# Performance work log

Measured on AMD Instinct MI355X. Metric: run time of the kernel, lower is better.

## Reference

```python
import jax, jax.numpy as jnp
import numpy as np

B, S, D, H, F = 8, 1024, 768, 12, 3072
DH = D // H
C_QUAD = 5.0
LN_EPS = 1e-5


def layer_norm(x, g, b):
    mu = jnp.mean(x, axis=-1, keepdims=True)
    var = jnp.mean(jnp.square(x - mu), axis=-1, keepdims=True)
    return (x - mu) * jax.lax.rsqrt(var + LN_EPS) * g + b


def setup_inputs() -> dict:
    key = jax.random.key(0)
    ks = jax.random.split(key, 8)
    s_in = 1.0 / np.sqrt(D)
    s_ff = 1.0 / np.sqrt(F)
    return {
        "x": jax.random.normal(ks[0], (B, S, D), jnp.float32),
        "wqkv": jax.random.normal(ks[1], (D, 3 * D), jnp.float32) * s_in,
        "bqkv": jnp.zeros((3 * D,), jnp.float32),
        "wo": jax.random.normal(ks[2], (D, D), jnp.float32) * s_in,
        "bo": jnp.zeros((D,), jnp.float32),
        "ln1_g": jnp.ones((D,), jnp.float32),
        "ln1_b": jnp.zeros((D,), jnp.float32),
        "w1": jax.random.normal(ks[3], (D, F), jnp.float32) * s_in,
        "b1": jnp.zeros((F,), jnp.float32),
        "w2": jax.random.normal(ks[4], (F, D), jnp.float32) * s_ff,
        "b2": jnp.zeros((D,), jnp.float32),
        "ln2_g": jnp.ones((D,), jnp.float32),
        "ln2_b": jnp.zeros((D,), jnp.float32),
    }


def quad2(scores):
    # Quad2 custom 'softmax': (s + c)^2 normalized by row sum
    s2 = jnp.square(scores + C_QUAD)
    return s2 / jnp.sum(s2, axis=-1, keepdims=True)


def reference(x, wqkv, bqkv, wo, bo, ln1_g, ln1_b, w1, b1, w2, b2, ln2_g, ln2_b):
    # --- pre-norm multi-head attention with Quad2 score normalization ---
    h = layer_norm(x, ln1_g, ln1_b)
    qkv = h @ wqkv + bqkv                              # [B,S,3D]
    q, k, v = jnp.split(qkv, 3, axis=-1)
    q = q.reshape(B, S, H, DH).transpose(0, 2, 1, 3)   # [B,H,S,Dh]
    k = k.reshape(B, S, H, DH).transpose(0, 2, 1, 3)
    v = v.reshape(B, S, H, DH).transpose(0, 2, 1, 3)
    scale = 1.0 / np.sqrt(DH)
    scores = jnp.einsum("bhqd,bhkd->bhqk", q, k) * scale
    attn = quad2(scores)                               # [B,H,S,S]
    ctx = jnp.einsum("bhqk,bhkd->bhqd", attn, v)
    ctx = ctx.transpose(0, 2, 1, 3).reshape(B, S, D)
    x = x + ctx @ wo + bo
    # --- pre-norm FFN ---
    h = layer_norm(x, ln2_g, ln2_b)
    h = jax.nn.gelu(h @ w1 + b1)
    x = x + h @ w2 + b2
    return x
```

## Files before the change

kernel.cpp:

```cpp
#include <hip/hip_runtime.h>
#include <hip/hip_bf16.h>

constexpr int B_ = 8;
constexpr int S_ = 1024;
constexpr int D_ = 768;
constexpr int H_ = 12;
constexpr int F_ = 3072;
constexpr int DH_ = 64;
constexpr int M_ = B_ * S_;
constexpr int PSZ = B_ * S_ * D_;

typedef __bf16 bf16x8 __attribute__((ext_vector_type(8)));
typedef float f32x4 __attribute__((ext_vector_type(4)));
typedef short s16x8 __attribute__((ext_vector_type(8)));
typedef short s16x4 __attribute__((ext_vector_type(4)));

__device__ __forceinline__ void gload_lds16(const __bf16* g, __bf16* l) {
    __builtin_amdgcn_global_load_lds(
        (const __attribute__((address_space(1))) void*)g,
        (__attribute__((address_space(3))) void*)l,
        16, 0, 0);
}

__device__ __forceinline__ float fast_gelu(float x) {
    float x3 = x * x * x;
    float z = 0.7978845608028654f * x + 0.035677408136300125f * x3;
    float e = __builtin_amdgcn_exp2f(-2.8853900817779268f * z);
    return x * __builtin_amdgcn_rcpf(1.0f + e);
}

__global__ __launch_bounds__(256) void transpose_cvt(const float* __restrict__ in,
                                                     __bf16* __restrict__ out,
                                                     int K, int N) {
    __shared__ float t[32][33];
    int tx = threadIdx.x, ty = threadIdx.y;
    int n0 = blockIdx.x * 32, k0 = blockIdx.y * 32;
#pragma unroll
    for (int i = 0; i < 4; ++i)
        t[ty + i * 8][tx] = in[(size_t)(k0 + ty + i * 8) * N + n0 + tx];
    __syncthreads();
#pragma unroll
    for (int i = 0; i < 4; ++i)
        out[(size_t)(n0 + ty + i * 8) * K + k0 + tx] = (__bf16)t[tx][ty + i * 8];
}

__global__ __launch_bounds__(256) void ln_kernel(const float* __restrict__ x,
                                                 const float* __restrict__ g,
                                                 const float* __restrict__ bb,
                                                 __bf16* __restrict__ out) {
    int row = blockIdx.x;
    const float* xr = x + (size_t)row * D_;
    int tid = threadIdx.x;
    float v[3];
    float s = 0.f, s2 = 0.f;
#pragma unroll
    for (int j = 0; j < 3; ++j) {
        v[j] = xr[tid + j * 256];
        s += v[j];
        s2 += v[j] * v[j];
    }
#pragma unroll
    for (int o = 32; o >= 1; o >>= 1) {
        s += __shfl_xor(s, o, 64);
        s2 += __shfl_xor(s2, o, 64);
    }
    __shared__ float red[8];
    int wid = tid >> 6, lane = tid & 63;
    if (lane == 0) { red[wid] = s; red[4 + wid] = s2; }
    __syncthreads();
    s = red[0] + red[1] + red[2] + red[3];
    s2 = red[4] + red[5] + red[6] + red[7];
    float mu = s * (1.0f / D_);
    float var = s2 * (1.0f / D_) - mu * mu;
    float rs = rsqrtf(var + 1e-5f);
    __bf16* orow = out + (size_t)row * D_;
#pragma unroll
    for (int j = 0; j < 3; ++j) {
        int i = tid + j * 256;
        orow[i] = (__bf16)((v[j] - mu) * rs * g[i] + bb[i]);
    }
}

template <int EPI>
__device__ __forceinline__ void gemm4_body(const __bf16* __restrict__ A,
                                           const __bf16* __restrict__ Bt,
                                           const float* __restrict__ bias,
                                           const float* __restrict__ res,
                                           float* __restrict__ outf,
                                           __bf16* __restrict__ outb,
                                           int M, int N, int K) {
    __shared__ __bf16 lds[2][16384];

    const int tid = threadIdx.x;
    const int lane = tid & 63, wid = tid >> 6;
    const int wm = wid >> 1, wn = wid & 1;
    const int gx = gridDim.x;
    const int nwg = gx * gridDim.y;
    int flat = blockIdx.y * gx + blockIdx.x;
    flat = (flat & 7) * (nwg >> 3) + (flat >> 3);
    const int bm = (flat / gx) * 128, bn = (flat % gx) * 128;
    const int l15 = lane & 15, l4 = lane >> 4;
    f32x4 acc[4][4] = {};

    const int r8 = tid >> 3;
    const int swc = ((tid & 7) ^ (r8 & 7)) * 8;
    const __bf16* ga = A + (size_t)(bm + r8) * K + swc;
    const __bf16* gb = Bt + (size_t)(bn + r8) * K + swc;
    const int NT = K / 64;

    auto stage = [&](int t, int s) {
        const int kt = t * 64;
        __bf16* base = &lds[s][0] + tid * 8;
#pragma unroll
        for (int j = 0; j < 4; ++j)
            gload_lds16(ga + kt + (size_t)j * 32 * K, base + j * 2048);
#pragma unroll
        for (int j = 0; j < 4; ++j)
            gload_lds16(gb + kt + (size_t)j * 32 * K, base + 8192 + j * 2048);
    };

    stage(0, 0);
    for (int t = 0; t < NT; ++t) {
        if (t + 1 < NT) {
            stage(t + 1, (t + 1) & 1);
            asm volatile("s_waitcnt vmcnt(8)" ::: "memory");
        } else {
            asm volatile("s_waitcnt vmcnt(0)" ::: "memory");
        }
        asm volatile("s_barrier" ::: "memory");

        const __bf16* sA = &lds[t & 1][0];
        const __bf16* sB = sA + 8192;
        const int swr = (l15 & 7) * 8;
        bf16x8 a[4][2], b[4][2];
#pragma unroll
        for (int mf = 0; mf < 4; ++mf) {
            int row = wm * 64 + mf * 16 + l15;
#pragma unroll
            for (int ks = 0; ks < 2; ++ks)
                a[mf][ks] = *(const bf16x8*)&sA[row * 64 + ((ks * 32 + l4 * 8) ^ swr)];
        }
#pragma unroll
        for (int nf = 0; nf < 4; ++nf) {
            int row = wn * 64 + nf * 16 + l15;
#pragma unroll
            for (int ks = 0; ks < 2; ++ks)
                b[nf][ks] = *(const bf16x8*)&sB[row * 64 + ((ks * 32 + l4 * 8) ^ swr)];
        }
        asm volatile("s_waitcnt lgkmcnt(0)" ::: "memory");
        asm volatile("s_barrier" ::: "memory");
        __builtin_amdgcn_sched_barrier(0);

        __builtin_amdgcn_s_setprio(1);
#pragma unroll
        for (int ks = 0; ks < 2; ++ks)
#pragma unroll
            for (int mf = 0; mf < 4; ++mf)
#pragma unroll
                for (int nf = 0; nf < 4; ++nf)
                    acc[mf][nf] = __builtin_amdgcn_mfma_f32_16x16x32_bf16(
                        a[mf][ks], b[nf][ks], acc[mf][nf], 0, 0, 0);
        __builtin_amdgcn_s_setprio(0);
    }

    if constexpr (EPI == 0) {
#pragma unroll
        for (int nf = 0; nf < 4; ++nf) {
            int n = bn + wn * 64 + nf * 16 + l15;
            int part = n / 768;
            int n7 = n - part * 768;
            float bv = bias[n];
            size_t obase = (size_t)part * PSZ + (size_t)(n7 >> 6) * (S_ * DH_) + (n7 & 63);
#pragma unroll
            for (int mf = 0; mf < 4; ++mf) {
                int m0 = bm + wm * 64 + mf * 16 + l4 * 4;
                size_t rb = obase + (size_t)(m0 >> 10) * ((size_t)H_ * S_ * DH_) +
                            (size_t)(m0 & 1023) * DH_;
#pragma unroll
                for (int r = 0; r < 4; ++r)
                    outb[rb + (size_t)r * DH_] = (__bf16)(acc[mf][nf][r] + bv);
            }
        }
    } else {
#pragma unroll
        for (int mf = 0; mf < 4; ++mf) {
#pragma unroll
            for (int nf = 0; nf < 4; ++nf) {
#pragma unroll
                for (int r = 0; r < 4; ++r) {
                    int m = bm + wm * 64 + mf * 16 + l4 * 4 + r;
                    int n = bn + wn * 64 + nf * 16 + l15;
                    float val = acc[mf][nf][r] + bias[n];
                    if constexpr (EPI == 1) {
                        outf[(size_t)m * N + n] = val + res[(size_t)m * N + n];
                    } else {
                        outb[(size_t)m * N + n] = (__bf16)fast_gelu(val);
                    }
                }
            }
        }
    }
}

template <int EPI>
__device__ __forceinline__ void gemmk_body(const __bf16* __restrict__ A,
                                           const __bf16* __restrict__ Bt,
                                           const float* __restrict__ bias,
                                           const float* __restrict__ res,
                                           float* __restrict__ outf,
                                           __bf16* __restrict__ outb,
                                           int M, int N, int K) {
    __shared__ __bf16 lds[2][16384];

    const int tid = threadIdx.x;
    const int lane = tid & 63, wid = tid >> 6;
    const int wm = wid >> 2, wn = wid & 3;
    const int gx = gridDim.x;
    const int nwg = gx * gridDim.y;
    int flat = blockIdx.y * gx + blockIdx.x;
    flat = (flat & 7) * (nwg >> 3) + (flat >> 3);
    const int bm = (flat / gx) * 128, bn = (flat % gx) * 128;
    const int l15 = lane & 15, l4 = lane >> 4;
    f32x4 acc[4][2] = {};

    const int r8 = tid >> 3;
    const int swc = ((tid & 7) ^ (r8 & 7)) * 8;
    const __bf16* ga = A + (size_t)(bm + r8) * K + swc;
    const __bf16* gb = Bt + (size_t)(bn + r8) * K + swc;
    const int NT = K / 64;

    auto stage = [&](int t, int s) {
        const int kt = t * 64;
        __bf16* base = &lds[s][0] + tid * 8;
        gload_lds16(ga + kt, base);
        gload_lds16(ga + kt + (size_t)64 * K, base + 4096);
        gload_lds16(gb + kt, base + 8192);
        gload_lds16(gb + kt + (size_t)64 * K, base + 12288);
    };

    stage(0, 0);
    for (int t = 0; t < NT; ++t) {
        if (t + 1 < NT) {
            stage(t + 1, (t + 1) & 1);
            asm volatile("s_waitcnt vmcnt(4)" ::: "memory");
        } else {
            asm volatile("s_waitcnt vmcnt(0)" ::: "memory");
        }
        asm volatile("s_barrier" ::: "memory");

        const __bf16* sA = &lds[t & 1][0];
        const __bf16* sB = sA + 8192;
        const int swr = (l15 & 7) * 8;
        bf16x8 a[4][2], b[2][2];
#pragma unroll
        for (int mf = 0; mf < 4; ++mf) {
            int row = wm * 64 + mf * 16 + l15;
#pragma unroll
            for (int ks = 0; ks < 2; ++ks)
                a[mf][ks] = *(const bf16x8*)&sA[row * 64 + ((ks * 32 + l4 * 8) ^ swr)];
        }
#pragma unroll
        for (int nf = 0; nf < 2; ++nf) {
            int row = wn * 32 + nf * 16 + l15;
#pragma unroll
            for (int ks = 0; ks < 2; ++ks)
                b[nf][ks] = *(const bf16x8*)&sB[row * 64 + ((ks * 32 + l4 * 8) ^ swr)];
        }
        asm volatile("s_waitcnt lgkmcnt(0)" ::: "memory");
        asm volatile("s_barrier" ::: "memory");
        __builtin_amdgcn_sched_barrier(0);

        __builtin_amdgcn_s_setprio(1);
#pragma unroll
        for (int ks = 0; ks < 2; ++ks)
#pragma unroll
            for (int mf = 0; mf < 4; ++mf)
#pragma unroll
                for (int nf = 0; nf < 2; ++nf)
                    acc[mf][nf] = __builtin_amdgcn_mfma_f32_16x16x32_bf16(
                        a[mf][ks], b[nf][ks], acc[mf][nf], 0, 0, 0);
        __builtin_amdgcn_s_setprio(0);
    }

#pragma unroll
    for (int mf = 0; mf < 4; ++mf) {
#pragma unroll
        for (int nf = 0; nf < 2; ++nf) {
#pragma unroll
            for (int r = 0; r < 4; ++r) {
                int m = bm + wm * 64 + mf * 16 + l4 * 4 + r;
                int n = bn + wn * 32 + nf * 16 + l15;
                float val = acc[mf][nf][r] + bias[n];
                if constexpr (EPI == 1) {
                    outf[(size_t)m * N + n] = val + res[(size_t)m * N + n];
                } else {
                    outb[(size_t)m * N + n] = (__bf16)fast_gelu(val);
                }
            }
        }
    }
    (void)outf;
}

__global__ __launch_bounds__(256) void g_qkv(const __bf16* A, const __bf16* Bt,
                                             const float* bias, __bf16* outb) {
    gemm4_body<0>(A, Bt, bias, nullptr, nullptr, outb, M_, 3 * D_, D_);
}
__global__ __launch_bounds__(256) void g_proj(const __bf16* A, const __bf16* Bt,
                                              const float* bias, const float* res,
                                              float* outf) {
    gemm4_body<1>(A, Bt, bias, res, outf, nullptr, M_, D_, D_);
}
__global__ __launch_bounds__(512) void g_ffn1(const __bf16* A, const __bf16* Bt,
                                              const float* bias, __bf16* outb) {
    gemmk_body<2>(A, Bt, bias, nullptr, nullptr, outb, M_, F_, D_);
}
__global__ __launch_bounds__(512) void g_ffn2(const __bf16* A, const __bf16* Bt,
                                              const float* bias, const float* res,
                                              float* outf) {
    gemmk_body<1>(A, Bt, bias, res, outf, nullptr, M_, D_, F_);
}

__global__ __launch_bounds__(256) void attn_kernel(const __bf16* __restrict__ qg,
                                                   const __bf16* __restrict__ kg,
                                                   const __bf16* __restrict__ vg,
                                                   __bf16* __restrict__ ctx) {
    __shared__ __bf16 Ks[64][72];
    __shared__ __bf16 Vt[64][72];
    __shared__ __bf16 Pw[4][32][72];
    __shared__ float den_l[4][32];
    int tid = threadIdx.x, lane = tid & 63, wid = tid >> 6;
    int l15 = lane & 15, l4 = lane >> 4;
    int idx = blockIdx.x;
    int xcd = idx & 7;
    int c = idx >> 3;
    int bh = xcd * 12 + (c >> 3);
    int qt = c & 7;
    int q0 = qt * 128;
    const __bf16* qbase = qg + (size_t)bh * S_ * DH_;
    const __bf16* kbase = kg + (size_t)bh * S_ * DH_;
    const __bf16* vbase = vg + (size_t)bh * S_ * DH_;

    int wq0 = q0 + wid * 32;
    bf16x8 qf[2][2];
#pragma unroll
    for (int qi = 0; qi < 2; ++qi)
#pragma unroll
        for (int ks = 0; ks < 2; ++ks)
            qf[qi][ks] = *(const bf16x8*)(qbase + (size_t)(wq0 + qi * 16 + l15) * DH_ +
                                          ks * 32 + l4 * 8);

    f32x4 oacc[2][4] = {};
    float den[2] = {0.f, 0.f};
    const float scale = 0.125f;

    for (int k0 = 0; k0 < S_; k0 += 64) {
        {
            int key = tid >> 2, dc = (tid & 3) * 16;
            *(s16x8*)&Ks[key][dc] =
                *(const s16x8*)(kbase + (size_t)(k0 + key) * DH_ + dc);
            *(s16x8*)&Ks[key][dc + 8] =
                *(const s16x8*)(kbase + (size_t)(k0 + key) * DH_ + dc + 8);
            int vkey = tid & 63, dg = (tid >> 6) * 16;
            s16x8 v0 = *(const s16x8*)(vbase + (size_t)(k0 + vkey) * DH_ + dg);
            s16x8 v1 = *(const s16x8*)(vbase + (size_t)(k0 + vkey) * DH_ + dg + 8);
#pragma unroll
            for (int e = 0; e < 8; ++e) {
                Vt[dg + e][vkey] = ((const __bf16*)&v0)[e];
                Vt[dg + 8 + e][vkey] = ((const __bf16*)&v1)[e];
            }
        }
        __syncthreads();

        bf16x8 kf[4][2];
#pragma unroll
        for (int kfi = 0; kfi < 4; ++kfi)
#pragma unroll
            for (int ks = 0; ks < 2; ++ks)
                kf[kfi][ks] = *(const bf16x8*)&Ks[kfi * 16 + l15][ks * 32 + l4 * 8];

#pragma unroll
        for (int qi = 0; qi < 2; ++qi) {
#pragma unroll
            for (int kfi = 0; kfi < 4; ++kfi) {
                f32x4 sa = {};
                sa = __builtin_amdgcn_mfma_f32_16x16x32_bf16(kf[kfi][0], qf[qi][0], sa, 0, 0, 0);
                sa = __builtin_amdgcn_mfma_f32_16x16x32_bf16(kf[kfi][1], qf[qi][1], sa, 0, 0, 0);
                __bf16 pk[4];
#pragma unroll
                for (int r = 0; r < 4; ++r) {
                    float p = sa[r] * scale + 5.0f;
                    p = p * p;
                    den[qi] += p;
                    pk[r] = (__bf16)p;
                }
                *(s16x4*)&Pw[wid][qi * 16 + l15][kfi * 16 + l4 * 4] =
                    *(const s16x4*)pk;
            }
        }

#pragma unroll
        for (int mf = 0; mf < 2; ++mf) {
#pragma unroll
            for (int ks = 0; ks < 2; ++ks) {
                bf16x8 pa = *(const bf16x8*)&Pw[wid][mf * 16 + l15][ks * 32 + l4 * 8];
#pragma unroll
                for (int nf = 0; nf < 4; ++nf) {
                    bf16x8 vb = *(const bf16x8*)&Vt[nf * 16 + l15][ks * 32 + l4 * 8];
                    oacc[mf][nf] = __builtin_amdgcn_mfma_f32_16x16x32_bf16(
                        pa, vb, oacc[mf][nf], 0, 0, 0);
                }
            }
        }
        __syncthreads();
    }

#pragma unroll
    for (int qi = 0; qi < 2; ++qi) {
        den[qi] += __shfl_xor(den[qi], 16, 64);
        den[qi] += __shfl_xor(den[qi], 32, 64);
    }
    if (lane < 16) {
        den_l[wid][lane] = den[0];
        den_l[wid][16 + lane] = den[1];
    }
    __syncthreads();

    int b_ = bh / H_, h_ = bh - b_ * H_;
#pragma unroll
    for (int mf = 0; mf < 2; ++mf)
#pragma unroll
        for (int nf = 0; nf < 4; ++nf) {
#pragma unroll
            for (int r = 0; r < 4; ++r) {
                int qrow = mf * 16 + l4 * 4 + r;
                int dcol = nf * 16 + l15;
                float val = oacc[mf][nf][r] *
                            __builtin_amdgcn_rcpf(den_l[wid][qrow]);
                int sI = q0 + wid * 32 + qrow;
                ctx[((size_t)b_ * S_ + sI) * D_ + h_ * DH_ + dcol] = (__bf16)val;
            }
        }
}

extern "C" void kernel_launch(void* const* d_in, const int* in_sizes, int n_in,
                              void* d_out, int out_size, void* d_ws, size_t ws_size,
                              hipStream_t stream) {
    const float* x    = (const float*)d_in[0];
    const float* wqkv = (const float*)d_in[1];
    const float* bqkv = (const float*)d_in[2];
    const float* wo   = (const float*)d_in[3];
    const float* bo   = (const float*)d_in[4];
    const float* ln1g = (const float*)d_in[5];
    const float* ln1b = (const float*)d_in[6];
    const float* w1   = (const float*)d_in[7];
    const float* b1   = (const float*)d_in[8];
    const float* w2   = (const float*)d_in[9];
    const float* b2   = (const float*)d_in[10];
    const float* ln2g = (const float*)d_in[11];
    const float* ln2b = (const float*)d_in[12];
    float* out = (float*)d_out;

    char* ws = (char*)d_ws;
    size_t off = 0;
    auto alloc = [&](size_t bytes) {
        void* p = ws + off;
        off += (bytes + 255) & ~(size_t)255;
        return p;
    };
    __bf16* wqkvT = (__bf16*)alloc((size_t)(3 * D_) * D_ * 2);
    __bf16* woT   = (__bf16*)alloc((size_t)D_ * D_ * 2);
    __bf16* w1T   = (__bf16*)alloc((size_t)F_ * D_ * 2);
    __bf16* w2T   = (__bf16*)alloc((size_t)D_ * F_ * 2);
    float*  X2    = (float*)alloc((size_t)M_ * D_ * 4);
    __bf16* Hb    = (__bf16*)alloc((size_t)M_ * D_ * 2);
    __bf16* Q3    = (__bf16*)alloc((size_t)4 * PSZ * 2);
    __bf16* Kb = Q3 + (size_t)PSZ;
    __bf16* Vb = Q3 + (size_t)2 * PSZ;
    __bf16* Cx = Q3 + (size_t)3 * PSZ;

    transpose_cvt<<<dim3((3 * D_) / 32, D_ / 32), dim3(32, 8), 0, stream>>>(wqkv, wqkvT, D_, 3 * D_);
    transpose_cvt<<<dim3(D_ / 32, D_ / 32), dim3(32, 8), 0, stream>>>(wo, woT, D_, D_);
    transpose_cvt<<<dim3(F_ / 32, D_ / 32), dim3(32, 8), 0, stream>>>(w1, w1T, D_, F_);
    transpose_cvt<<<dim3(D_ / 32, F_ / 32), dim3(32, 8), 0, stream>>>(w2, w2T, F_, D_);

    ln_kernel<<<M_, 256, 0, stream>>>(x, ln1g, ln1b, Hb);
    g_qkv<<<dim3((3 * D_) / 128, M_ / 128), 256, 0, stream>>>(Hb, wqkvT, bqkv, Q3);
    attn_kernel<<<B_ * H_ * (S_ / 128), 256, 0, stream>>>(Q3, Kb, Vb, Cx);
    g_proj<<<dim3(D_ / 128, M_ / 128), 256, 0, stream>>>(Cx, woT, bo, x, X2);
    ln_kernel<<<M_, 256, 0, stream>>>(X2, ln2g, ln2b, Hb);
    g_ffn1<<<dim3(F_ / 128, M_ / 128), 512, 0, stream>>>(Hb, w1T, b1, Q3);
    g_ffn2<<<dim3(D_ / 128, M_ / 128), 512, 0, stream>>>(Q3, w2T, b2, X2, out);
    (void)in_sizes; (void)n_in; (void)out_size; (void)ws_size;
}
```

Before: 226.1 us.

## Retile GEMMs, use 128x64 tiles for residual GEMMs, pipeline attention K/V loads

The GEMM wrappers become templated global kernels. The projection and FFN2 GEMMs use a new 128x64-tile, 256-thread kernel, which doubles their block count for better CU fill. FFN1 moves from the 512-thread 128x128 kernel to the 4-wave 128x128 kernel. The attention kernel drops the XCD-aware block remap and prefetches the next K/V tile into registers while computing the current one, using raw barriers. These changes trade per-block reuse for parallelism, and the remap removal may hurt L2 locality.

```diff
diff --git a/kernel.cpp b/kernel.cpp
--- a/kernel.cpp
+++ b/kernel.cpp
@@ -82,13 +82,13 @@
 }
 
 template <int EPI>
-__device__ __forceinline__ void gemm4_body(const __bf16* __restrict__ A,
-                                           const __bf16* __restrict__ Bt,
-                                           const float* __restrict__ bias,
-                                           const float* __restrict__ res,
-                                           float* __restrict__ outf,
-                                           __bf16* __restrict__ outb,
-                                           int M, int N, int K) {
+__global__ __launch_bounds__(256) void gemm4(const __bf16* __restrict__ A,
+                                             const __bf16* __restrict__ Bt,
+                                             const float* __restrict__ bias,
+                                             const float* __restrict__ res,
+                                             float* __restrict__ outf,
+                                             __bf16* __restrict__ outb,
+                                             int M, int N, int K) {
     __shared__ __bf16 lds[2][16384];
 
     const int tid = threadIdx.x;
@@ -200,26 +200,26 @@
             }
         }
     }
+    (void)res; (void)outf;
 }
 
 template <int EPI>
-__device__ __forceinline__ void gemmk_body(const __bf16* __restrict__ A,
-                                           const __bf16* __restrict__ Bt,
-                                           const float* __restrict__ bias,
-                                           const float* __restrict__ res,
-                                           float* __restrict__ outf,
-                                           __bf16* __restrict__ outb,
-                                           int M, int N, int K) {
-    __shared__ __bf16 lds[2][16384];
+__global__ __launch_bounds__(256) void gemm64(const __bf16* __restrict__ A,
+                                              const __bf16* __restrict__ Bt,
+                                              const float* __restrict__ bias,
+                                              const float* __restrict__ res,
+                                              float* __restrict__ outf,
+                                              int M, int N, int K) {
+    __shared__ __bf16 lds[2][12288];
 
     const int tid = threadIdx.x;
     const int lane = tid & 63, wid = tid >> 6;
-    const int wm = wid >> 2, wn = wid & 3;
+    const int wm = wid >> 1, wn = wid & 1;
     const int gx = gridDim.x;
     const int nwg = gx * gridDim.y;
     int flat = blockIdx.y * gx + blockIdx.x;
     flat = (flat & 7) * (nwg >> 3) + (flat >> 3);
-    const int bm = (flat / gx) * 128, bn = (flat % gx) * 128;
+    const int bm = (flat / gx) * 128, bn = (flat % gx) * 64;
     const int l15 = lane & 15, l4 = lane >> 4;
     f32x4 acc[4][2] = {};
 
@@ -232,17 +232,19 @@
     auto stage = [&](int t, int s) {
         const int kt = t * 64;
         __bf16* base = &lds[s][0] + tid * 8;
-        gload_lds16(ga + kt, base);
-        gload_lds16(ga + kt + (size_t)64 * K, base + 4096);
-        gload_lds16(gb + kt, base + 8192);
-        gload_lds16(gb + kt + (size_t)64 * K, base + 12288);
+#pragma unroll
+        for (int j = 0; j < 4; ++j)
+            gload_lds16(ga + kt + (size_t)j * 32 * K, base + j * 2048);
+#pragma unroll
+        for (int j = 0; j < 2; ++j)
+            gload_lds16(gb + kt + (size_t)j * 32 * K, base + 8192 + j * 2048);
     };
 
     stage(0, 0);
     for (int t = 0; t < NT; ++t) {
         if (t + 1 < NT) {
             stage(t + 1, (t + 1) & 1);
-            asm volatile("s_waitcnt vmcnt(4)" ::: "memory");
+            asm volatile("s_waitcnt vmcnt(6)" ::: "memory");
         } else {
             asm volatile("s_waitcnt vmcnt(0)" ::: "memory");
         }
@@ -290,35 +292,11 @@
             for (int r = 0; r < 4; ++r) {
                 int m = bm + wm * 64 + mf * 16 + l4 * 4 + r;
                 int n = bn + wn * 32 + nf * 16 + l15;
-                float val = acc[mf][nf][r] + bias[n];
-                if constexpr (EPI == 1) {
-                    outf[(size_t)m * N + n] = val + res[(size_t)m * N + n];
-                } else {
-                    outb[(size_t)m * N + n] = (__bf16)fast_gelu(val);
-                }
-            }
-        }
-    }
-    (void)outf;
-}
-
-__global__ __launch_bounds__(256) void g_qkv(const __bf16* A, const __bf16* Bt,
-                                             const float* bias, __bf16* outb) {
-    gemm4_body<0>(A, Bt, bias, nullptr, nullptr, outb, M_, 3 * D_, D_);
-}
-__global__ __launch_bounds__(256) void g_proj(const __bf16* A, const __bf16* Bt,
-                                              const float* bias, const float* res,
-                                              float* outf) {
-    gemm4_body<1>(A, Bt, bias, res, outf, nullptr, M_, D_, D_);
-}
-__global__ __launch_bounds__(512) void g_ffn1(const __bf16* A, const __bf16* Bt,
-                                              const float* bias, __bf16* outb) {
-    gemmk_body<2>(A, Bt, bias, nullptr, nullptr, outb, M_, F_, D_);
-}
-__global__ __launch_bounds__(512) void g_ffn2(const __bf16* A, const __bf16* Bt,
-                                              const float* bias, const float* res,
-                                              float* outf) {
-    gemmk_body<1>(A, Bt, bias, res, outf, nullptr, M_, D_, F_);
+                outf[(size_t)m * N + n] =
+                    acc[mf][nf][r] + bias[n] + res[(size_t)m * N + n];
+            }
+        }
+    }
 }
 
 __global__ __launch_bounds__(256) void attn_kernel(const __bf16* __restrict__ qg,
@@ -331,11 +309,7 @@
     __shared__ float den_l[4][32];
     int tid = threadIdx.x, lane = tid & 63, wid = tid >> 6;
     int l15 = lane & 15, l4 = lane >> 4;
-    int idx = blockIdx.x;
-    int xcd = idx & 7;
-    int c = idx >> 3;
-    int bh = xcd * 12 + (c >> 3);
-    int qt = c & 7;
+    int bh = blockIdx.x >> 3, qt = blockIdx.x & 7;
     int q0 = qt * 128;
     const __bf16* qbase = qg + (size_t)bh * S_ * DH_;
     const __bf16* kbase = kg + (size_t)bh * S_ * DH_;
@@ -354,23 +328,31 @@
     float den[2] = {0.f, 0.f};
     const float scale = 0.125f;
 
-    for (int k0 = 0; k0 < S_; k0 += 64) {
-        {
-            int key = tid >> 2, dc = (tid & 3) * 16;
-            *(s16x8*)&Ks[key][dc] =
-                *(const s16x8*)(kbase + (size_t)(k0 + key) * DH_ + dc);
-            *(s16x8*)&Ks[key][dc + 8] =
-                *(const s16x8*)(kbase + (size_t)(k0 + key) * DH_ + dc + 8);
-            int vkey = tid & 63, dg = (tid >> 6) * 16;
-            s16x8 v0 = *(const s16x8*)(vbase + (size_t)(k0 + vkey) * DH_ + dg);
-            s16x8 v1 = *(const s16x8*)(vbase + (size_t)(k0 + vkey) * DH_ + dg + 8);
-#pragma unroll
-            for (int e = 0; e < 8; ++e) {
-                Vt[dg + e][vkey] = ((const __bf16*)&v0)[e];
-                Vt[dg + 8 + e][vkey] = ((const __bf16*)&v1)[e];
-            }
-        }
-        __syncthreads();
+    const int key = tid >> 2, dc = (tid & 3) * 16;
+    const int vkey = tid & 63, dg = (tid >> 6) * 16;
+    s16x8 kA, kB, vA, vB;
+
+    auto load_regs = [&](int t) {
+        int k0 = t * 64;
+        kA = *(const s16x8*)(kbase + (size_t)(k0 + key) * DH_ + dc);
+        kB = *(const s16x8*)(kbase + (size_t)(k0 + key) * DH_ + dc + 8);
+        vA = *(const s16x8*)(vbase + (size_t)(k0 + vkey) * DH_ + dg);
+        vB = *(const s16x8*)(vbase + (size_t)(k0 + vkey) * DH_ + dg + 8);
+    };
+
+    load_regs(0);
+    for (int t = 0; t < 16; ++t) {
+        asm volatile("s_barrier" ::: "memory");
+        *(s16x8*)&Ks[key][dc] = kA;
+        *(s16x8*)&Ks[key][dc + 8] = kB;
+#pragma unroll
+        for (int e = 0; e < 8; ++e) {
+            Vt[dg + e][vkey] = ((const __bf16*)&vA)[e];
+            Vt[dg + 8 + e][vkey] = ((const __bf16*)&vB)[e];
+        }
+        if (t + 1 < 16) load_regs(t + 1);
+        asm volatile("s_waitcnt lgkmcnt(0)" ::: "memory");
+        asm volatile("s_barrier" ::: "memory");
 
         bf16x8 kf[4][2];
 #pragma unroll
@@ -412,7 +394,6 @@
                 }
             }
         }
-        __syncthreads();
     }
 
 #pragma unroll
@@ -420,6 +401,7 @@
         den[qi] += __shfl_xor(den[qi], 16, 64);
         den[qi] += __shfl_xor(den[qi], 32, 64);
     }
+    __syncthreads();
     if (lane < 16) {
         den_l[wid][lane] = den[0];
         den_l[wid][16 + lane] = den[1];
@@ -485,11 +467,15 @@
     transpose_cvt<<<dim3(D_ / 32, F_ / 32), dim3(32, 8), 0, stream>>>(w2, w2T, F_, D_);
 
     ln_kernel<<<M_, 256, 0, stream>>>(x, ln1g, ln1b, Hb);
-    g_qkv<<<dim3((3 * D_) / 128, M_ / 128), 256, 0, stream>>>(Hb, wqkvT, bqkv, Q3);
+    gemm4<0><<<dim3((3 * D_) / 128, M_ / 128), 256, 0, stream>>>(
+        Hb, wqkvT, bqkv, nullptr, nullptr, Q3, M_, 3 * D_, D_);
     attn_kernel<<<B_ * H_ * (S_ / 128), 256, 0, stream>>>(Q3, Kb, Vb, Cx);
-    g_proj<<<dim3(D_ / 128, M_ / 128), 256, 0, stream>>>(Cx, woT, bo, x, X2);
+    gemm64<1><<<dim3(D_ / 64, M_ / 128), 256, 0, stream>>>(
+        Cx, woT, bo, x, X2, M_, D_, D_);
     ln_kernel<<<M_, 256, 0, stream>>>(X2, ln2g, ln2b, Hb);
-    g_ffn1<<<dim3(F_ / 128, M_ / 128), 512, 0, stream>>>(Hb, w1T, b1, Q3);
-    g_ffn2<<<dim3(D_ / 128, M_ / 128), 512, 0, stream>>>(Q3, w2T, b2, X2, out);
+    gemm4<2><<<dim3(F_ / 128, M_ / 128), 256, 0, stream>>>(
+        Hb, w1T, b1, nullptr, nullptr, Q3, M_, F_, D_);
+    gemm64<1><<<dim3(D_ / 64, M_ / 128), 256, 0, stream>>>(
+        Q3, w2T, b2, X2, out, M_, D_, F_);
     (void)in_sizes; (void)n_in; (void)out_size; (void)ws_size;
 }
```

Result: no change. 226.5 us (+0.2%).
